# Performance work log

Measured on AMD Instinct MI355X. Metric: run time of the kernel, lower is better.

## Reference

```python
import jax, jax.numpy as jnp
import numpy as np

N = 50000   # nodes
E = 800000  # edges
D = 128     # node_channels


def setup_inputs() -> dict:
    key = jax.random.key(0)
    ks = jax.random.split(key, 16)
    s = 1.0 / np.sqrt(D)
    inp = {
        "x": jax.random.normal(ks[0], (N, D), dtype=jnp.float32),
        "edge_index": jax.random.randint(ks[1], (2, E), 0, N, dtype=jnp.int64),
        "eps": jax.random.normal(ks[2], (N, D), dtype=jnp.float32),
    }
    names = ["1", "2", "mu", "logstd", "5", "6"]
    for i, nm in enumerate(names):
        inp[f"W{nm}"] = jax.random.normal(ks[3 + 2 * i], (D, D), dtype=jnp.float32) * s
        inp[f"b{nm}"] = jnp.zeros((D,), dtype=jnp.float32)
    return inp


def _gcn_norm(edge_index, num_nodes):
    # add self-loops, then symmetric normalization deg^{-1/2} (A+I) deg^{-1/2}
    loop = jnp.arange(num_nodes, dtype=edge_index.dtype)
    src = jnp.concatenate([edge_index[0], loop])
    dst = jnp.concatenate([edge_index[1], loop])
    deg = jax.ops.segment_sum(jnp.ones_like(src, dtype=jnp.float32), dst,
                              num_segments=num_nodes)
    dis = jnp.where(deg > 0, jax.lax.rsqrt(deg), 0.0)
    norm = dis[src] * dis[dst]  # [E + N]
    return src, dst, norm


def _gcn(x, W, b, src, dst, norm, num_nodes):
    h = x @ W                              # [N, D] small GEMM
    msg = h[src] * norm[:, None]           # gather + scale, [E+N, D]
    out = jax.ops.segment_sum(msg, dst, num_segments=num_nodes)  # scatter-add
    return out + b


def reference(x, edge_index, eps, W1, b1, W2, b2, Wmu, bmu, Wlogstd, blogstd,
              W5, b5, W6, b6):
    num_nodes = x.shape[0]
    src, dst, norm = _gcn_norm(edge_index, num_nodes)
    g = lambda h, W, b: _gcn(h, W, b, src, dst, norm, num_nodes)

    nodes = jax.nn.relu(g(x, W1, b1))
    nodes = jax.nn.relu(g(nodes, W2, b2))
    mu = g(nodes, Wmu, bmu)
    logstd = g(nodes, Wlogstd, blogstd)
    # reparametrize (training mode), divider = 10
    nodes = mu + eps * jnp.exp(logstd) / 10.0
    nodes = jax.nn.relu(g(nodes, W5, b5))
    nodes = jax.nn.relu(g(nodes, W6, b6))
    return nodes
```

## Files before the change

### kernel.cpp

```cpp
#include <hip/hip_runtime.h>
#include <hip/hip_bf16.h>
#include <cstdint>
#include <cstddef>

#define D 128
#define NWG 200

typedef _Float16 f16;
typedef f16 f16x2 __attribute__((ext_vector_type(2)));
typedef f16 f16x4 __attribute__((ext_vector_type(4)));
typedef f16 f16x8 __attribute__((ext_vector_type(8)));
typedef float f32x4 __attribute__((ext_vector_type(4)));

static inline size_t align256(size_t x){ return (x + 255) & ~(size_t)255; }

__global__ void detect_kernel(const int* __restrict__ ei, long long n32, int* __restrict__ flag){
  __shared__ int s;
  if (threadIdx.x == 0) s = 0;
  __syncthreads();
  int nz = 0;
  for (long long i = 2LL*threadIdx.x + 1; i < 4096 && i < n32; i += 512)
    nz |= (ei[i] != 0);
  if (nz) s = 1;
  __syncthreads();
  if (threadIdx.x == 0) *flag = (s ? 0 : 1);
}

__device__ __forceinline__ void load_edge(const void* ei, int E, int is64, int e, int& s, int& d){
  if (is64) {
    const long long* p = (const long long*)ei;
    s = (int)p[e]; d = (int)p[(size_t)E + e];
  } else {
    const int* p = (const int*)ei;
    s = p[e]; d = p[(size_t)E + e];
  }
}

__global__ __launch_bounds__(256) void passA_hist(
    const void* __restrict__ ei, int E, const int* __restrict__ flag,
    int* __restrict__ glob_hist, int NB){
  __shared__ int cnt[256];
  int t = threadIdx.x, wg = blockIdx.x;
  cnt[t] = 0;
  __syncthreads();
  int is64 = *flag;
  int chunk = (E + NWG - 1) / NWG;
  int lo = wg * chunk, hi = min(lo + chunk, E);
  for (int e = lo + t; e < hi; e += 256){
    int s, d;
    load_edge(ei, E, is64, e, s, d);
    atomicAdd(&cnt[d >> 8], 1);
  }
  __syncthreads();
  for (int b = t; b < NB; b += 256)
    glob_hist[b * NWG + wg] = cnt[b];
}

__global__ void scan_partial(const int* __restrict__ src, int* __restrict__ dst,
                             int* __restrict__ blockSums, int L){
  __shared__ int sd[256];
  int t = threadIdx.x;
  int base = blockIdx.x * 1024 + t * 4;
  int v[4]; int s = 0;
  #pragma unroll
  for (int j = 0; j < 4; ++j){ v[j] = (base + j < L) ? src[base + j] : 0; s += v[j]; }
  sd[t] = s; __syncthreads();
  for (int off = 1; off < 256; off <<= 1){
    int x = (t >= off) ? sd[t - off] : 0;
    __syncthreads();
    sd[t] += x;
    __syncthreads();
  }
  int run = sd[t] - s;
  #pragma unroll
  for (int j = 0; j < 4; ++j){
    if (base + j < L) dst[base + j] = run;
    run += v[j];
  }
  if (t == 255) blockSums[blockIdx.x] = sd[255];
}

__global__ void scan_blocksums(int* __restrict__ blockSums, int nblk,
                               int* __restrict__ dst, int L, int total){
  __shared__ int sd[256];
  int t = threadIdx.x;
  int v = (t < nblk) ? blockSums[t] : 0;
  sd[t] = v; __syncthreads();
  for (int off = 1; off < 256; off <<= 1){
    int x = (t >= off) ? sd[t - off] : 0;
    __syncthreads();
    sd[t] += x;
    __syncthreads();
  }
  if (t < nblk) blockSums[t] = sd[t] - v;
  if (t == 0) dst[L] = total;
}

__global__ void scan_add(int* __restrict__ dst, const int* __restrict__ blockSums, int L){
  int i = blockIdx.x * blockDim.x + threadIdx.x;
  if (i >= L) return;
  dst[i] += blockSums[i >> 10];
}

__global__ __launch_bounds__(256) void passB_scatter(
    const void* __restrict__ ei, int E, const int* __restrict__ flag,
    const int* __restrict__ bucketOff, int NB, unsigned* __restrict__ packed){
  __shared__ int cur[256];
  int t = threadIdx.x, wg = blockIdx.x;
  for (int b = t; b < NB; b += 256)
    cur[b] = bucketOff[b * NWG + wg];
  __syncthreads();
  int is64 = *flag;
  int chunk = (E + NWG - 1) / NWG;
  int lo = wg * chunk, hi = min(lo + chunk, E);
  for (int e = lo + t; e < hi; e += 256){
    int s, d;
    load_edge(ei, E, is64, e, s, d);
    int pos = atomicAdd(&cur[d >> 8], 1);
    packed[pos] = (unsigned)s | ((unsigned)(d & 255) << 16);
  }
}

__global__ __launch_bounds__(256) void passC_csr(
    const unsigned* __restrict__ packed, const int* __restrict__ bucketOff,
    int NB, int N, int E,
    int* __restrict__ rowptr, float* __restrict__ dis, int* __restrict__ csr_src){
  __shared__ int degl[256];
  __shared__ int sd[256];
  __shared__ int cur[256];
  int t = threadIdx.x, b = blockIdx.x;
  int begin = bucketOff[(size_t)b * NWG];
  int endb  = bucketOff[(size_t)(b + 1) * NWG];
  degl[t] = 0;
  __syncthreads();
  for (int i = begin + t; i < endb; i += 256)
    atomicAdd(&degl[(packed[i] >> 16) & 255], 1);
  __syncthreads();
  int dv = degl[t];
  sd[t] = dv; __syncthreads();
  for (int off = 1; off < 256; off <<= 1){
    int x = (t >= off) ? sd[t - off] : 0;
    __syncthreads();
    sd[t] += x;
    __syncthreads();
  }
  int localOff = sd[t] - dv;
  int v = b * 256 + t;
  if (v < N){
    rowptr[v] = begin + localOff;
    dis[v] = rsqrtf((float)(dv + 1));
  }
  if (b == NB - 1 && t == 0) rowptr[N] = E;
  cur[t] = begin + localOff;
  __syncthreads();
  for (int i = begin + t; i < endb; i += 256){
    unsigned p = packed[i];
    int pos = atomicAdd(&cur[(p >> 16) & 255], 1);
    csr_src[pos] = (int)(p & 0xFFFFu);
  }
}

__global__ void cast_scale(const float* __restrict__ in, const float* __restrict__ dis,
                           f16* __restrict__ out, int n4){
  int i = blockIdx.x * blockDim.x + threadIdx.x;
  if (i >= n4) return;
  float dv = dis[i >> 5];
  float4 v = ((const float4*)in)[i];
  f16x4 o; o[0]=(f16)(v.x*dv); o[1]=(f16)(v.y*dv); o[2]=(f16)(v.z*dv); o[3]=(f16)(v.w*dv);
  ((f16x4*)out)[i] = o;
}

__global__ void prep_w(const float* __restrict__ Wa, const float* __restrict__ Wb,
                       const float* __restrict__ Wc, const float* __restrict__ Wd,
                       const float* __restrict__ We, const float* __restrict__ Wf,
                       f16* __restrict__ Wt){
  int i = blockIdx.x * 256 + threadIdx.x;
  int w = i >> 14, rem = i & 16383;
  int n = rem >> 7, k = rem & 127;
  const float* Wp = (w==0)?Wa:(w==1)?Wb:(w==2)?Wc:(w==3)?Wd:(w==4)?We:Wf;
  Wt[i] = (f16)Wp[k*128 + n];
}

__global__ __launch_bounds__(256) void agg16(
    const f16* __restrict__ in, f16* __restrict__ out,
    const int* __restrict__ rowptr, const int* __restrict__ csr_src,
    const float* __restrict__ dis, int N){
  int v = blockIdx.x * 4 + (threadIdx.x >> 6);
  if (v >= N) return;
  int c2 = (threadIdx.x & 63) * 2;
  float dv = dis[v];
  int beg = rowptr[v], end = rowptr[v + 1];
  f16x2 sv = *(const f16x2*)&in[(size_t)v * D + c2];
  float acc0 = (float)sv[0], acc1 = (float)sv[1];
  int e = beg;
  for (; e + 3 < end; e += 4){
    int u0 = csr_src[e],     u1 = csr_src[e + 1];
    int u2 = csr_src[e + 2], u3 = csr_src[e + 3];
    f16x2 h0 = *(const f16x2*)&in[(size_t)u0 * D + c2];
    f16x2 h1 = *(const f16x2*)&in[(size_t)u1 * D + c2];
    f16x2 h2 = *(const f16x2*)&in[(size_t)u2 * D + c2];
    f16x2 h3 = *(const f16x2*)&in[(size_t)u3 * D + c2];
    acc0 += (float)h0[0] + (float)h1[0] + (float)h2[0] + (float)h3[0];
    acc1 += (float)h0[1] + (float)h1[1] + (float)h2[1] + (float)h3[1];
  }
  for (; e < end; ++e){
    int u = csr_src[e];
    f16x2 h = *(const f16x2*)&in[(size_t)u * D + c2];
    acc0 += (float)h[0]; acc1 += (float)h[1];
  }
  f16x2 o; o[0] = (f16)(acc0 * dv); o[1] = (f16)(acc1 * dv);
  *(f16x2*)&out[(size_t)v * D + c2] = o;
}

template<int EPI>
__global__ __launch_bounds__(256) void gemm_mfma(
    const f16* __restrict__ A, const f16* __restrict__ Wt, const float* __restrict__ bias,
    const f16* __restrict__ Wt2, const float* __restrict__ bias2,
    const float* __restrict__ eps, const float* __restrict__ dis,
    f16* __restrict__ out16, float* __restrict__ outf, int N){

  extern __shared__ __align__(16) f16 Ws[];

  int t = threadIdx.x;
  {
    int r = t & 127, p = t >> 7;
    const float4* src = (const float4*)&Wt[r * 128 + p * 64];
    f16* dstrow = &Ws[r * 128];
    #pragma unroll
    for (int i = 0; i < 8; ++i){
      int q = p * 8 + i;
      *(float4*)&dstrow[(q ^ (r & 7)) * 8] = src[i];
    }
    if (EPI == 1){
      const float4* src2 = (const float4*)&Wt2[r * 128 + p * 64];
      f16* dstrow2 = &Ws[16384 + r * 128];
      #pragma unroll
      for (int i = 0; i < 8; ++i){
        int q = p * 8 + i;
        *(float4*)&dstrow2[(q ^ (r & 7)) * 8] = src2[i];
      }
    }
  }
  __syncthreads();

  int wave = t >> 6, lane = t & 63;
  int r0 = blockIdx.x * 64 + wave * 16;
  int lrow = lane & 15, hi = lane >> 4;

  int rr = min(r0 + lrow, N - 1);
  const f16* arow = &A[(size_t)rr * D + hi * 8];
  f16x8 a[4];
  #pragma unroll
  for (int s = 0; s < 4; ++s) a[s] = *(const f16x8*)&arow[s * 32];

  f32x4 acc[8] = {};
  f32x4 acc2[8] = {};

  #pragma unroll
  for (int s = 0; s < 4; ++s){
    #pragma unroll
    for (int tt = 0; tt < 8; ++tt){
      int n = tt * 16 + lrow;
      int q = (s * 4 + hi) ^ (lrow & 7);
      f16x8 b = *(const f16x8*)&Ws[n * 128 + q * 8];
      acc[tt] = __builtin_amdgcn_mfma_f32_16x16x32_f16(a[s], b, acc[tt], 0, 0, 0);
      if (EPI == 1){
        f16x8 b2 = *(const f16x8*)&Ws[16384 + n * 128 + q * 8];
        acc2[tt] = __builtin_amdgcn_mfma_f32_16x16x32_f16(a[s], b2, acc2[tt], 0, 0, 0);
      }
    }
  }

  int orow0 = r0 + hi * 4;
  #pragma unroll
  for (int tt = 0; tt < 8; ++tt){
    int col = tt * 16 + lrow;
    float bv = bias[col];
    float bv2 = (EPI == 1) ? bias2[col] : 0.f;
    #pragma unroll
    for (int i = 0; i < 4; ++i){
      int r = orow0 + i;
      if (r >= N) continue;
      float v = acc[tt][i] + bv;
      if (EPI == 0){
        out16[(size_t)r * D + col] = (f16)(fmaxf(v, 0.f) * dis[r]);
      } else if (EPI == 1){
        float ls = acc2[tt][i] + bv2;
        float z = v + eps[(size_t)r * D + col] * __expf(ls) * 0.1f;
        out16[(size_t)r * D + col] = (f16)(z * dis[r]);
      } else {
        outf[(size_t)r * D + col] = fmaxf(v, 0.f);
      }
    }
  }
}

extern "C" void kernel_launch(void* const* d_in, const int* in_sizes, int n_in,
                              void* d_out, int out_size, void* d_ws, size_t ws_size,
                              hipStream_t stream){
  const float* x   = (const float*)d_in[0];
  const void*  ei  = d_in[1];
  const float* eps = (const float*)d_in[2];
  const float* W1  = (const float*)d_in[3];  const float* b1  = (const float*)d_in[4];
  const float* W2  = (const float*)d_in[5];  const float* b2  = (const float*)d_in[6];
  const float* Wmu = (const float*)d_in[7];  const float* bmu = (const float*)d_in[8];
  const float* Wls = (const float*)d_in[9];  const float* bls = (const float*)d_in[10];
  const float* W5  = (const float*)d_in[11]; const float* b5  = (const float*)d_in[12];
  const float* W6  = (const float*)d_in[13]; const float* b6  = (const float*)d_in[14];

  const int N = in_sizes[0] / D;
  const int E = in_sizes[1] / 2;
  const int NB = (N + 255) >> 8;
  const int L  = NB * NWG;
  float* out = (float*)d_out;

  char* ws = (char*)d_ws;
  size_t off = 0;
  auto alloc = [&](size_t bytes){ char* p = ws + off; off += align256(bytes); return p; };
  int*      flag      = (int*)     alloc(256);
  int*      glob_hist = (int*)     alloc(((size_t)L + 1) * 4);
  int*      bucketOff = (int*)     alloc(((size_t)L + 1) * 4);
  int*      blockSums = (int*)     alloc(1024);
  int*      rowptr    = (int*)     alloc(((size_t)N + 1) * 4);
  float*    dis       = (float*)   alloc((size_t)N * 4);
  unsigned* packed    = (unsigned*)alloc((size_t)E * 4);
  int*      csr_src   = (int*)     alloc((size_t)E * 4);
  f16*      Wt        = (f16*)     alloc((size_t)6 * 128 * 128 * 2);
  f16*      bufA      = (f16*)     alloc((size_t)N * D * 2);
  f16*      bufB      = (f16*)     alloc((size_t)N * D * 2);
  (void)ws_size; (void)n_in; (void)out_size;

  detect_kernel<<<1, 256, 0, stream>>>((const int*)ei, (long long)2 * E, flag);

  passA_hist<<<NWG, 256, 0, stream>>>(ei, E, flag, glob_hist, NB);
  int nblk = (L + 1023) / 1024;
  scan_partial<<<nblk, 256, 0, stream>>>(glob_hist, bucketOff, blockSums, L);
  scan_blocksums<<<1, 256, 0, stream>>>(blockSums, nblk, bucketOff, L, E);
  scan_add<<<(L + 255) / 256, 256, 0, stream>>>(bucketOff, blockSums, L);
  passB_scatter<<<NWG, 256, 0, stream>>>(ei, E, flag, bucketOff, NB, packed);
  passC_csr<<<NB, 256, 0, stream>>>(packed, bucketOff, NB, N, E, rowptr, dis, csr_src);

  cast_scale<<<(N * D / 4 + 255) / 256, 256, 0, stream>>>(x, dis, bufB, N * D / 4);
  prep_w<<<(6 * 16384) / 256, 256, 0, stream>>>(W1, W2, Wmu, Wls, W5, W6, Wt);

  int aggGrid = (N + 3) / 4;
  int gemmGrid = (N + 63) / 64;
  size_t lds1 = 128 * 128 * sizeof(f16);
  size_t lds2 = 2 * 128 * 128 * sizeof(f16);

  agg16<<<aggGrid, 256, 0, stream>>>(bufB, bufA, rowptr, csr_src, dis, N);
  gemm_mfma<0><<<gemmGrid, 256, lds1, stream>>>(bufA, Wt + 0*16384, b1, nullptr, nullptr, nullptr, dis, bufB, nullptr, N);
  agg16<<<aggGrid, 256, 0, stream>>>(bufB, bufA, rowptr, csr_src, dis, N);
  gemm_mfma<0><<<gemmGrid, 256, lds1, stream>>>(bufA, Wt + 1*16384, b2, nullptr, nullptr, nullptr, dis, bufB, nullptr, N);
  agg16<<<aggGrid, 256, 0, stream>>>(bufB, bufA, rowptr, csr_src, dis, N);
  gemm_mfma<1><<<gemmGrid, 256, lds2, stream>>>(bufA, Wt + 2*16384, bmu, Wt + 3*16384, bls, eps, dis, bufB, nullptr, N);
  agg16<<<aggGrid, 256, 0, stream>>>(bufB, bufA, rowptr, csr_src, dis, N);
  gemm_mfma<0><<<gemmGrid, 256, lds1, stream>>>(bufA, Wt + 4*16384, b5, nullptr, nullptr, nullptr, dis, bufB, nullptr, N);
  agg16<<<aggGrid, 256, 0, stream>>>(bufB, bufA, rowptr, csr_src, dis, N);
  gemm_mfma<2><<<gemmGrid, 256, lds1, stream>>>(bufA, Wt + 5*16384, b6, nullptr, nullptr, nullptr, dis, nullptr, out, N);
}
```

Measured before the change: 457.0 us.

## Deepen gather unroll in aggregation and vectorize GEMM epilogue with transposed MFMA

The aggregation kernel now issues eight independent neighbor gathers per iteration instead of four, giving more loads in flight. The GEMM kernel moves to 512-thread blocks covering 128 rows, so each weight tile staged in LDS is reused by twice as many rows. It also issues the A-row loads before the LDS weight fill so the two overlap. Swapping the MFMA operands transposes the output fragment, so each lane owns one row and four contiguous columns, which lets bias, eps and output use 4-wide vector loads and stores instead of scalar strided ones. The cost is higher register pressure in the aggregation loop and fewer, larger GEMM blocks.

```diff
diff --git a/kernel.cpp b/kernel.cpp
--- a/kernel.cpp
+++ b/kernel.cpp
@@ -193,17 +193,24 @@
   f16x2 sv = *(const f16x2*)&in[(size_t)v * D + c2];
   float acc0 = (float)sv[0], acc1 = (float)sv[1];
   int e = beg;
-  for (; e + 3 < end; e += 4){
-    int u0 = csr_src[e],     u1 = csr_src[e + 1];
-    int u2 = csr_src[e + 2], u3 = csr_src[e + 3];
+  for (; e + 7 < end; e += 8){
+    f16x2 h[8];
+    #pragma unroll
+    for (int j = 0; j < 8; ++j){
+      int u = csr_src[e + j];
+      h[j] = *(const f16x2*)&in[(size_t)u * D + c2];
+    }
+    #pragma unroll
+    for (int j = 0; j < 8; ++j){ acc0 += (float)h[j][0]; acc1 += (float)h[j][1]; }
+  }
+  for (; e + 1 < end; e += 2){
+    int u0 = csr_src[e], u1 = csr_src[e + 1];
     f16x2 h0 = *(const f16x2*)&in[(size_t)u0 * D + c2];
     f16x2 h1 = *(const f16x2*)&in[(size_t)u1 * D + c2];
-    f16x2 h2 = *(const f16x2*)&in[(size_t)u2 * D + c2];
-    f16x2 h3 = *(const f16x2*)&in[(size_t)u3 * D + c2];
-    acc0 += (float)h0[0] + (float)h1[0] + (float)h2[0] + (float)h3[0];
-    acc1 += (float)h0[1] + (float)h1[1] + (float)h2[1] + (float)h3[1];
-  }
-  for (; e < end; ++e){
+    acc0 += (float)h0[0] + (float)h1[0];
+    acc1 += (float)h0[1] + (float)h1[1];
+  }
+  if (e < end){
     int u = csr_src[e];
     f16x2 h = *(const f16x2*)&in[(size_t)u * D + c2];
     acc0 += (float)h[0]; acc1 += (float)h[1];
@@ -213,7 +220,7 @@
 }
 
 template<int EPI>
-__global__ __launch_bounds__(256) void gemm_mfma(
+__global__ __launch_bounds__(512) void gemm_mfma(
     const f16* __restrict__ A, const f16* __restrict__ Wt, const float* __restrict__ bias,
     const f16* __restrict__ Wt2, const float* __restrict__ bias2,
     const float* __restrict__ eps, const float* __restrict__ dis,
@@ -222,36 +229,40 @@
   extern __shared__ __align__(16) f16 Ws[];
 
   int t = threadIdx.x;
+  int wave = t >> 6, lane = t & 63;
+  int lrow = lane & 15, hi = lane >> 4;
+  int r0 = blockIdx.x * 128 + wave * 16;
+  bool active = (r0 < N);
+
+  f16x8 a[4];
+  if (active){
+    int rr = min(r0 + lrow, N - 1);
+    const f16* arow = &A[(size_t)rr * D + hi * 8];
+    #pragma unroll
+    for (int s = 0; s < 4; ++s) a[s] = *(const f16x8*)&arow[s * 32];
+  }
+
   {
     int r = t & 127, p = t >> 7;
-    const float4* src = (const float4*)&Wt[r * 128 + p * 64];
+    const float4* src = (const float4*)&Wt[r * 128 + p * 32];
     f16* dstrow = &Ws[r * 128];
     #pragma unroll
-    for (int i = 0; i < 8; ++i){
-      int q = p * 8 + i;
+    for (int i = 0; i < 4; ++i){
+      int q = p * 4 + i;
       *(float4*)&dstrow[(q ^ (r & 7)) * 8] = src[i];
     }
     if (EPI == 1){
-      const float4* src2 = (const float4*)&Wt2[r * 128 + p * 64];
+      const float4* src2 = (const float4*)&Wt2[r * 128 + p * 32];
       f16* dstrow2 = &Ws[16384 + r * 128];
       #pragma unroll
-      for (int i = 0; i < 8; ++i){
-        int q = p * 8 + i;
+      for (int i = 0; i < 4; ++i){
+        int q = p * 4 + i;
         *(float4*)&dstrow2[(q ^ (r & 7)) * 8] = src2[i];
       }
     }
   }
   __syncthreads();
-
-  int wave = t >> 6, lane = t & 63;
-  int r0 = blockIdx.x * 64 + wave * 16;
-  int lrow = lane & 15, hi = lane >> 4;
-
-  int rr = min(r0 + lrow, N - 1);
-  const f16* arow = &A[(size_t)rr * D + hi * 8];
-  f16x8 a[4];
-  #pragma unroll
-  for (int s = 0; s < 4; ++s) a[s] = *(const f16x8*)&arow[s * 32];
+  if (!active) return;
 
   f32x4 acc[8] = {};
   f32x4 acc2[8] = {};
@@ -263,34 +274,45 @@
       int n = tt * 16 + lrow;
       int q = (s * 4 + hi) ^ (lrow & 7);
       f16x8 b = *(const f16x8*)&Ws[n * 128 + q * 8];
-      acc[tt] = __builtin_amdgcn_mfma_f32_16x16x32_f16(a[s], b, acc[tt], 0, 0, 0);
+      acc[tt] = __builtin_amdgcn_mfma_f32_16x16x32_f16(b, a[s], acc[tt], 0, 0, 0);
       if (EPI == 1){
         f16x8 b2 = *(const f16x8*)&Ws[16384 + n * 128 + q * 8];
-        acc2[tt] = __builtin_amdgcn_mfma_f32_16x16x32_f16(a[s], b2, acc2[tt], 0, 0, 0);
+        acc2[tt] = __builtin_amdgcn_mfma_f32_16x16x32_f16(b2, a[s], acc2[tt], 0, 0, 0);
       }
     }
   }
 
-  int orow0 = r0 + hi * 4;
+  int r = r0 + lrow;
+  if (r >= N) return;
+  float dv = (EPI == 2) ? 1.f : dis[r];
+  int cbase = hi * 4;
   #pragma unroll
   for (int tt = 0; tt < 8; ++tt){
-    int col = tt * 16 + lrow;
-    float bv = bias[col];
-    float bv2 = (EPI == 1) ? bias2[col] : 0.f;
-    #pragma unroll
-    for (int i = 0; i < 4; ++i){
-      int r = orow0 + i;
-      if (r >= N) continue;
-      float v = acc[tt][i] + bv;
-      if (EPI == 0){
-        out16[(size_t)r * D + col] = (f16)(fmaxf(v, 0.f) * dis[r]);
-      } else if (EPI == 1){
-        float ls = acc2[tt][i] + bv2;
-        float z = v + eps[(size_t)r * D + col] * __expf(ls) * 0.1f;
-        out16[(size_t)r * D + col] = (f16)(z * dis[r]);
-      } else {
-        outf[(size_t)r * D + col] = fmaxf(v, 0.f);
+    int n0 = tt * 16 + cbase;
+    f32x4 bv = *(const f32x4*)&bias[n0];
+    if (EPI == 0){
+      f16x4 o;
+      #pragma unroll
+      for (int ii = 0; ii < 4; ++ii)
+        o[ii] = (f16)(fmaxf(acc[tt][ii] + bv[ii], 0.f) * dv);
+      *(f16x4*)&out16[(size_t)r * D + n0] = o;
+    } else if (EPI == 1){
+      f32x4 bv2 = *(const f32x4*)&bias2[n0];
+      f32x4 e4  = *(const f32x4*)&eps[(size_t)r * D + n0];
+      f16x4 o;
+      #pragma unroll
+      for (int ii = 0; ii < 4; ++ii){
+        float mu = acc[tt][ii] + bv[ii];
+        float ls = acc2[tt][ii] + bv2[ii];
+        o[ii] = (f16)((mu + e4[ii] * __expf(ls) * 0.1f) * dv);
       }
+      *(f16x4*)&out16[(size_t)r * D + n0] = o;
+    } else {
+      f32x4 o;
+      #pragma unroll
+      for (int ii = 0; ii < 4; ++ii)
+        o[ii] = fmaxf(acc[tt][ii] + bv[ii], 0.f);
+      *(f32x4*)&outf[(size_t)r * D + n0] = o;
     }
   }
 }
@@ -344,18 +366,18 @@
   prep_w<<<(6 * 16384) / 256, 256, 0, stream>>>(W1, W2, Wmu, Wls, W5, W6, Wt);
 
   int aggGrid = (N + 3) / 4;
-  int gemmGrid = (N + 63) / 64;
+  int gemmGrid = (N + 127) / 128;
   size_t lds1 = 128 * 128 * sizeof(f16);
   size_t lds2 = 2 * 128 * 128 * sizeof(f16);
 
   agg16<<<aggGrid, 256, 0, stream>>>(bufB, bufA, rowptr, csr_src, dis, N);
-  gemm_mfma<0><<<gemmGrid, 256, lds1, stream>>>(bufA, Wt + 0*16384, b1, nullptr, nullptr, nullptr, dis, bufB, nullptr, N);
-  agg16<<<aggGrid, 256, 0, stream>>>(bufB, bufA, rowptr, csr_src, dis, N);
-  gemm_mfma<0><<<gemmGrid, 256, lds1, stream>>>(bufA, Wt + 1*16384, b2, nullptr, nullptr, nullptr, dis, bufB, nullptr, N);
-  agg16<<<aggGrid, 256, 0, stream>>>(bufB, bufA, rowptr, csr_src, dis, N);
-  gemm_mfma<1><<<gemmGrid, 256, lds2, stream>>>(bufA, Wt + 2*16384, bmu, Wt + 3*16384, bls, eps, dis, bufB, nullptr, N);
-  agg16<<<aggGrid, 256, 0, stream>>>(bufB, bufA, rowptr, csr_src, dis, N);
-  gemm_mfma<0><<<gemmGrid, 256, lds1, stream>>>(bufA, Wt + 4*16384, b5, nullptr, nullptr, nullptr, dis, bufB, nullptr, N);
-  agg16<<<aggGrid, 256, 0, stream>>>(bufB, bufA, rowptr, csr_src, dis, N);
-  gemm_mfma<2><<<gemmGrid, 256, lds1, stream>>>(bufA, Wt + 5*16384, b6, nullptr, nullptr, nullptr, dis, nullptr, out, N);
-}
+  gemm_mfma<0><<<gemmGrid, 512, lds1, stream>>>(bufA, Wt + 0*16384, b1, nullptr, nullptr, nullptr, dis, bufB, nullptr, N);
+  agg16<<<aggGrid, 256, 0, stream>>>(bufB, bufA, rowptr, csr_src, dis, N);
+  gemm_mfma<0><<<gemmGrid, 512, lds1, stream>>>(bufA, Wt + 1*16384, b2, nullptr, nullptr, nullptr, dis, bufB, nullptr, N);
+  agg16<<<aggGrid, 256, 0, stream>>>(bufB, bufA, rowptr, csr_src, dis, N);
+  gemm_mfma<1><<<gemmGrid, 512, lds2, stream>>>(bufA, Wt + 2*16384, bmu, Wt + 3*16384, bls, eps, dis, bufB, nullptr, N);
+  agg16<<<aggGrid, 256, 0, stream>>>(bufB, bufA, rowptr, csr_src, dis, N);
+  gemm_mfma<0><<<gemmGrid, 512, lds1, stream>>>(bufA, Wt + 4*16384, b5, nullptr, nullptr, nullptr, dis, bufB, nullptr, N);
+  agg16<<<aggGrid, 256, 0, stream>>>(bufB, bufA, rowptr, csr_src, dis, N);
+  gemm_mfma<2><<<gemmGrid, 512, lds1, stream>>>(bufA, Wt + 5*16384, b6, nullptr, nullptr, nullptr, dis, nullptr, out, N);
+}
```

Result: faster. 396.6 us (-13.2%).
